# Kernel optimization log

Hardware: AMD Instinct MI355X
Metric: run time of the kernel (lower is better)

## Reference

```python
import jax, jax.numpy as jnp
import numpy as np

SHAPES = [(76, 76), (38, 38), (19, 19), (1, 20)]  # 3 feature levels + task-token pseudo-level
D, HEADS, NLVL, NPTS = 256, 8, 4, 4
DH = D // HEADS
NLAYERS = 6
B = 2
S = sum(h * w for h, w in SHAPES)  # 7601


def _ref_points():
    # valid_ratios == 1 (no padding) -> normalized pixel-center grid per level, concatenated. [S,2] (x,y)
    refs = []
    for H, W in SHAPES:
        ry, rx = jnp.meshgrid(jnp.linspace(0.5, H - 0.5, H) / H,
                              jnp.linspace(0.5, W - 0.5, W) / W, indexing='ij')
        refs.append(jnp.stack([rx.ravel(), ry.ravel()], -1))
    return jnp.concatenate(refs, 0)


def _layer_norm(x, g, b):
    m = x.mean(-1, keepdims=True)
    v = ((x - m) ** 2).mean(-1, keepdims=True)
    return (x - m) * jax.lax.rsqrt(v + 1e-5) * g + b


def _bilinear(val_l, locx, locy, H, W):
    # val_l: [B, H*W, HEADS, DH]; locx/locy: [B,Q,HEADS,P] normalized coords.
    # grid_sample semantics: align_corners=False, zero padding.
    v = val_l.transpose(0, 2, 1, 3)  # [B,Hh,HW,DH]
    x = locx * W - 0.5
    y = locy * H - 0.5
    x0 = jnp.floor(x)
    y0 = jnp.floor(y)
    wx1 = x - x0
    wy1 = y - y0

    def corner(xi, yi, w):
        valid = ((xi >= 0) & (xi <= W - 1) & (yi >= 0) & (yi <= H - 1)).astype(v.dtype)
        idx = (jnp.clip(yi, 0, H - 1) * W + jnp.clip(xi, 0, W - 1)).astype(jnp.int32)
        idx_t = idx.transpose(0, 2, 1, 3)  # [B,Hh,Q,P]
        Bq, Hh, Q, P = idx_t.shape
        g = jnp.take_along_axis(v, idx_t.reshape(Bq, Hh, Q * P)[..., None], axis=2)
        g = g.reshape(Bq, Hh, Q, P, DH)
        return g * (w * valid).transpose(0, 2, 1, 3)[..., None]

    return (corner(x0, y0, (1 - wx1) * (1 - wy1)) + corner(x0 + 1, y0, wx1 * (1 - wy1))
            + corner(x0, y0 + 1, (1 - wx1) * wy1) + corner(x0 + 1, y0 + 1, wx1 * wy1))


def _msdeform(q, x, ref, Woff, boff, Wa, ba, Wv, bv, Wo, bo):
    Bq, Sq, _ = x.shape
    value = (x @ Wv + bv).reshape(Bq, Sq, HEADS, DH)
    off = (q @ Woff + boff).reshape(Bq, Sq, HEADS, NLVL, NPTS, 2)
    attn = jax.nn.softmax((q @ Wa + ba).reshape(Bq, Sq, HEADS, NLVL * NPTS), -1)
    attn = attn.reshape(Bq, Sq, HEADS, NLVL, NPTS)
    acc = jnp.zeros((Bq, HEADS, Sq, DH), x.dtype)
    start = 0
    for l, (H, W) in enumerate(SHAPES):
        n = H * W
        loc = ref[None, :, None, None, :] + off[:, :, :, l] / jnp.asarray([W, H], x.dtype)
        samp = _bilinear(value[:, start:start + n], loc[..., 0], loc[..., 1], H, W)  # [B,Hh,S,P,DH]
        a = attn[:, :, :, l].transpose(0, 2, 1, 3)  # [B,Hh,S,P]
        acc = acc + (samp * a[..., None]).sum(3)
        start += n
    return acc.transpose(0, 2, 1, 3).reshape(Bq, Sq, D) @ Wo + bo


def reference(src0, src1, src2, pos0, pos1, pos2, task_encoding, task_pos_enc, level_embed,
              W_off, b_off, W_attn, b_attn, W_val, b_val, W_out, b_out,
              W1, b1, W2, b2, g1, beta1, g2, beta2):
    srcs, poss = [src0, src1, src2], [pos0, pos1, pos2]
    sf, pf = [], []
    for l in range(3):
        Bq, C, H, W = srcs[l].shape
        sf.append(srcs[l].reshape(Bq, C, H * W).transpose(0, 2, 1))
        pf.append(poss[l].reshape(Bq, C, H * W).transpose(0, 2, 1) + level_embed[l])
    sf.append(task_encoding)
    pf.append(jnp.broadcast_to(task_pos_enc[None], task_encoding.shape))
    x = jnp.concatenate(sf, 1)   # [B,S,D]
    pos = jnp.concatenate(pf, 1)
    ref = _ref_points()
    for i in range(NLAYERS):
        q = x + pos
        x = _layer_norm(x + _msdeform(q, x, ref, W_off[i], b_off[i], W_attn[i], b_attn[i],
                                      W_val[i], b_val[i], W_out[i], b_out[i]), g1[i], beta1[i])
        x = _layer_norm(x + jax.nn.relu(x @ W1[i] + b1[i]) @ W2[i] + b2[i], g2[i], beta2[i])
    return x


def setup_inputs() -> dict:
    key = jax.random.key(0)
    ks = jax.random.split(key, 20)
    d = {}
    for i, (H, W) in enumerate(SHAPES[:3]):
        d[f'src{i}'] = jax.random.normal(ks[i], (B, D, H, W), jnp.float32)
        d[f'pos{i}'] = jax.random.normal(ks[3 + i], (B, D, H, W), jnp.float32) * 0.1
    d['task_encoding'] = jax.random.normal(ks[6], (B, 20, D), jnp.float32)
    d['task_pos_enc'] = jax.random.normal(ks[7], (20, D), jnp.float32) * 0.1
    d['level_embed'] = jax.random.normal(ks[8], (NLVL, D), jnp.float32) * 0.1

    def w(k, shape, s=0.02):
        return jax.random.normal(k, shape, jnp.float32) * s

    d['W_off'] = w(ks[9], (NLAYERS, D, HEADS * NLVL * NPTS * 2), 0.01)
    d['b_off'] = w(ks[10], (NLAYERS, HEADS * NLVL * NPTS * 2), 0.2)
    d['W_attn'] = w(ks[11], (NLAYERS, D, HEADS * NLVL * NPTS))
    d['b_attn'] = jnp.zeros((NLAYERS, HEADS * NLVL * NPTS), jnp.float32)
    d['W_val'] = w(ks[12], (NLAYERS, D, D))
    d['b_val'] = jnp.zeros((NLAYERS, D), jnp.float32)
    d['W_out'] = w(ks[13], (NLAYERS, D, D))
    d['b_out'] = jnp.zeros((NLAYERS, D), jnp.float32)
    d['W1'] = w(ks[14], (NLAYERS, D, 2048))
    d['b1'] = jnp.zeros((NLAYERS, 2048), jnp.float32)
    d['W2'] = w(ks[15], (NLAYERS, 2048, D))
    d['b2'] = jnp.zeros((NLAYERS, D), jnp.float32)
    d['g1'] = jnp.ones((NLAYERS, D), jnp.float32)
    d['beta1'] = jnp.zeros((NLAYERS, D), jnp.float32)
    d['g2'] = jnp.ones((NLAYERS, D), jnp.float32)
    d['beta2'] = jnp.zeros((NLAYERS, D), jnp.float32)
    return d
```

## Files before the change

kernel.cpp:

```cpp
#include <hip/hip_runtime.h>

#define S_TOT 7601
#define BATCH 2
#define BM (BATCH * S_TOT)
#define DMODEL 256

typedef unsigned short bf16;
typedef __attribute__((ext_vector_type(8))) short v8s;
typedef __attribute__((ext_vector_type(4))) float v4f;

__device__ __forceinline__ float b2f(bf16 u) {
    union { unsigned int i; float f; } v;
    v.i = ((unsigned int)u) << 16;
    return v.f;
}
__device__ __forceinline__ bf16 f2b(float f) {
    union { unsigned int i; float f; } v;
    v.f = f;
    unsigned int r = v.i + 0x7FFFu + ((v.i >> 16) & 1u);
    return (bf16)(r >> 16);
}
__device__ __forceinline__ float ldin(const void* p, size_t i, int isf32) {
    return isf32 ? ((const float*)p)[i] : b2f(((const bf16*)p)[i]);
}

#define GLDS16(gp, lp)                                                          \
    __builtin_amdgcn_global_load_lds(                                           \
        (const __attribute__((address_space(1))) unsigned int*)(gp),            \
        (__attribute__((address_space(3))) unsigned int*)(lp), 16, 0, 0)

__device__ __forceinline__ void xcd_remap(int& bx, int& by) {
    int gx = gridDim.x, gy = gridDim.y;
    int nwg = gx * gy;
    int lin = blockIdx.y * gx + blockIdx.x;
    int q = nwg >> 3, r = nwg & 7;
    int xcd = lin & 7, idx = lin >> 3;
    int lin2 = (xcd < r ? xcd * (q + 1) : r * (q + 1) + (xcd - r) * q) + idx;
    bx = lin2 % gx;
    by = lin2 / gx;
}

__global__ void detect_dtype(const unsigned short* __restrict__ src, int* __restrict__ flag) {
    __shared__ int cnt;
    if (threadIdx.x == 0) cnt = 0;
    __syncthreads();
    int local = 0;
    for (int i = threadIdx.x; i < 16384; i += 256) {
        unsigned int e = (src[i] >> 7) & 0xFFu;
        if (e >= 143u) local++;
    }
    atomicAdd(&cnt, local);
    __syncthreads();
    if (threadIdx.x == 0) *flag = (cnt > 200) ? 1 : 0;
}

__global__ void __launch_bounds__(256) pack_level(const void* __restrict__ src,
                                                  const void* __restrict__ pin,
                                                  const void* __restrict__ lemb, int lrow,
                                                  float* __restrict__ x,
                                                  bf16* __restrict__ pout,
                                                  int HW, int start,
                                                  const int* __restrict__ flag) {
    int isf32 = *flag;
    int i = blockIdx.x * 256 + threadIdx.x;
    int total = BATCH * HW * 256;
    if (i >= total) return;
    int c = i & 255;
    int t = i >> 8;
    int s = t % HW;
    int b = t / HW;
    size_t src_idx = ((size_t)b * 256 + c) * HW + s;
    float sv = ldin(src, src_idx, isf32);
    float pv = ldin(pin, src_idx, isf32) + ldin(lemb, (size_t)lrow * 256 + c, isf32);
    size_t o = ((size_t)b * S_TOT + start + s) * 256 + c;
    x[o] = sv;
    pout[o] = f2b(pv);
}

__global__ void __launch_bounds__(256) pack_task(const void* __restrict__ te,
                                                 const void* __restrict__ tpe,
                                                 float* __restrict__ x,
                                                 bf16* __restrict__ pout,
                                                 const int* __restrict__ flag) {
    int isf32 = *flag;
    int i = blockIdx.x * 256 + threadIdx.x;
    int total = BATCH * 20 * 256;
    if (i >= total) return;
    int c = i & 255;
    int t = (i >> 8) % 20;
    int b = (i >> 8) / 20;
    size_t o = ((size_t)b * S_TOT + 7581 + t) * 256 + c;
    x[o] = ldin(te, ((size_t)b * 20 + t) * 256 + c, isf32);
    pout[o] = f2b(ldin(tpe, (size_t)t * 256 + c, isf32));
}

__global__ void __launch_bounds__(256) make_ref(float* __restrict__ ref) {
    int s = blockIdx.x * 256 + threadIdx.x;
    if (s >= S_TOT) return;
    int H, W, st;
    if (s < 5776)      { H = 76; W = 76; st = 0; }
    else if (s < 7220) { H = 38; W = 38; st = 5776; }
    else if (s < 7581) { H = 19; W = 19; st = 7220; }
    else               { H = 1;  W = 20; st = 7581; }
    int r = s - st;
    int i = r / W, j = r % W;
    ref[s * 2 + 0] = (j + 0.5f) / (float)W;
    ref[s * 2 + 1] = (i + 0.5f) / (float)H;
}

__global__ void __launch_bounds__(256) cast_out(const float* __restrict__ x,
                                                void* __restrict__ o, int n,
                                                const int* __restrict__ flag) {
    int isf32 = *flag;
    int i = blockIdx.x * 256 + threadIdx.x;
    if (i >= n) return;
    if (isf32) ((float*)o)[i] = x[i];
    else       ((bf16*)o)[i] = f2b(x[i]);
}

__global__ void __launch_bounds__(256) cvt_x(const float* __restrict__ x,
                                             bf16* __restrict__ xb, int n4) {
    int i = blockIdx.x * 256 + threadIdx.x;
    if (i >= n4) return;
    float4 xv = ((const float4*)x)[i];
    ushort4 xo;
    xo.x = f2b(xv.x); xo.y = f2b(xv.y); xo.z = f2b(xv.z); xo.w = f2b(xv.w);
    ((ushort4*)xb)[i] = xo;
}

__global__ void __launch_bounds__(256) cvt_q(const float* __restrict__ x,
                                             const bf16* __restrict__ pos,
                                             bf16* __restrict__ qb, int n4) {
    int i = blockIdx.x * 256 + threadIdx.x;
    if (i >= n4) return;
    float4 xv = ((const float4*)x)[i];
    ushort4 pv = ((const ushort4*)pos)[i];
    ushort4 qo;
    qo.x = f2b(xv.x + b2f(pv.x));
    qo.y = f2b(xv.y + b2f(pv.y));
    qo.z = f2b(xv.z + b2f(pv.z));
    qo.w = f2b(xv.w + b2f(pv.w));
    ((ushort4*)qb)[i] = qo;
}

__global__ void __launch_bounds__(256) transpose_all(const void* __restrict__ Wv,
                                                     const void* __restrict__ Woff,
                                                     const void* __restrict__ Wa,
                                                     const void* __restrict__ Wo,
                                                     const void* __restrict__ W1,
                                                     const void* __restrict__ W2,
                                                     bf16* __restrict__ Wvt,
                                                     bf16* __restrict__ Wofft,
                                                     bf16* __restrict__ Wat,
                                                     bf16* __restrict__ Wot,
                                                     bf16* __restrict__ W1t,
                                                     bf16* __restrict__ W2t,
                                                     int L, const int* __restrict__ flag) {
    int isf32 = *flag;
    int t = blockIdx.x;
    const void* src; bf16* dst; int K, N; size_t woff;
    if (t < 64)        { src = Wv;   dst = Wvt;   K = 256;  N = 256;  woff = (size_t)L * 65536; }
    else if (t < 128)  { src = Woff; dst = Wofft; K = 256;  N = 256;  woff = (size_t)L * 65536;  t -= 64; }
    else if (t < 160)  { src = Wa;   dst = Wat;   K = 256;  N = 128;  woff = (size_t)L * 32768;  t -= 128; }
    else if (t < 224)  { src = Wo;   dst = Wot;   K = 256;  N = 256;  woff = (size_t)L * 65536;  t -= 160; }
    else if (t < 736)  { src = W1;   dst = W1t;   K = 256;  N = 2048; woff = (size_t)L * 524288; t -= 224; }
    else               { src = W2;   dst = W2t;   K = 2048; N = 256;  woff = (size_t)L * 524288; t -= 736; }
    int ntx = N >> 5;
    int tk = (t / ntx) * 32;
    int tn = (t % ntx) * 32;
    __shared__ float tl[32][33];
    int r = threadIdx.x >> 3;
    int c4 = (threadIdx.x & 7) * 4;
#pragma unroll
    for (int i = 0; i < 4; ++i)
        tl[r][c4 + i] = ldin(src, woff + (size_t)(tk + r) * N + tn + c4 + i, isf32);
    __syncthreads();
#pragma unroll
    for (int i = 0; i < 4; ++i)
        dst[(size_t)(tn + r) * K + tk + c4 + i] = f2b(tl[c4 + i][r]);
}

__global__ void __launch_bounds__(256) mfma_gemm(const bf16* __restrict__ A,
                                                 const bf16* __restrict__ Wt,
                                                 const void* __restrict__ bias, size_t boff,
                                                 bf16* __restrict__ C,
                                                 int M, int N, int K, int relu,
                                                 const int* __restrict__ flag) {
    int isf32 = *flag;
    __shared__ __align__(16) char smem[128 * 136 * 2];
    bf16* Cs = (bf16*)smem;
    int tid = threadIdx.x;
    int lane = tid & 63, wave = tid >> 6;
    int wm = (wave & 1) << 6, wn = (wave >> 1) << 6;
    int bx, by;
    xcd_remap(bx, by);
    int bm = by * 128, bn = bx * 128;
    int q = lane >> 4, l15 = lane & 15;

    v4f acc[4][4];
#pragma unroll
    for (int i = 0; i < 4; ++i)
#pragma unroll
        for (int j = 0; j < 4; ++j) acc[i][j] = (v4f){0.f, 0.f, 0.f, 0.f};

    int r0 = tid >> 2;
    int oct = (tid & 3) * 8;
    int am0 = bm + r0;      if (am0 >= M) am0 = M - 1;
    int am1 = bm + r0 + 64; if (am1 >= M) am1 = M - 1;
    const bf16* ag0 = A + (size_t)am0 * K + oct;
    const bf16* ag1 = A + (size_t)am1 * K + oct;
    const bf16* bg0 = Wt + (size_t)(bn + r0) * K + oct;
    const bf16* bg1 = Wt + (size_t)(bn + r0 + 64) * K + oct;

    int NT = K >> 5;
    {
        bf16* base = (bf16*)smem;
        GLDS16(ag0, base + tid * 8);
        GLDS16(ag1, base + (tid + 256) * 8);
        GLDS16(bg0, base + 4096 + tid * 8);
        GLDS16(bg1, base + 4096 + (tid + 256) * 8);
    }
    __syncthreads();
    for (int it = 0; it < NT; ++it) {
        if (it + 1 < NT) {
            bf16* base = (bf16*)smem + ((it + 1) & 1) * 8192;
            int k0 = (it + 1) << 5;
            GLDS16(ag0 + k0, base + tid * 8);
            GLDS16(ag1 + k0, base + (tid + 256) * 8);
            GLDS16(bg0 + k0, base + 4096 + tid * 8);
            GLDS16(bg1 + k0, base + 4096 + (tid + 256) * 8);
        }
        const bf16* As = (const bf16*)smem + (it & 1) * 8192;
        const bf16* Bs = As + 4096;
        v8s a_frag[4], b_frag[4];
#pragma unroll
        for (int mi = 0; mi < 4; ++mi)
            a_frag[mi] = *(const v8s*)&As[(wm + mi * 16 + l15) * 32 + q * 8];
#pragma unroll
        for (int ni = 0; ni < 4; ++ni)
            b_frag[ni] = *(const v8s*)&Bs[(wn + ni * 16 + l15) * 32 + q * 8];
#pragma unroll
        for (int mi = 0; mi < 4; ++mi)
#pragma unroll
            for (int ni = 0; ni < 4; ++ni)
                acc[mi][ni] = __builtin_amdgcn_mfma_f32_16x16x32_bf16(
                    a_frag[mi], b_frag[ni], acc[mi][ni], 0, 0, 0);
        __syncthreads();
    }

#pragma unroll
    for (int ni = 0; ni < 4; ++ni) {
        int cn = wn + ni * 16 + l15;
        float bv = ldin(bias, boff + bn + cn, isf32);
#pragma unroll
        for (int mi = 0; mi < 4; ++mi) {
#pragma unroll
            for (int r = 0; r < 4; ++r) {
                float v = acc[mi][ni][r] + bv;
                if (relu) v = fmaxf(v, 0.f);
                Cs[(wm + mi * 16 + q * 4 + r) * 136 + cn] = f2b(v);
            }
        }
    }
    __syncthreads();
    {
        int row = tid >> 1, half = tid & 1;
        int gm = bm + row;
        if (gm < M) {
            const bf16* srcp = Cs + row * 136 + half * 64;
            bf16* dstp = C + (size_t)gm * N + bn + half * 64;
#pragma unroll
            for (int i = 0; i < 8; ++i)
                *(uint4*)(dstp + i * 8) = *(const uint4*)(srcp + i * 8);
        }
    }
}

__global__ void __launch_bounds__(256) mfma_gemm64(const bf16* __restrict__ A,
                                                   const bf16* __restrict__ Wt,
                                                   const void* __restrict__ bias, size_t boff,
                                                   bf16* __restrict__ C,
                                                   int M, int N, int K, int relu,
                                                   const int* __restrict__ flag) {
    int isf32 = *flag;
    __shared__ __align__(16) char smem[16384];
    bf16* Cs = (bf16*)smem;
    int tid = threadIdx.x;
    int lane = tid & 63, wave = tid >> 6;
    int wm = (wave & 1) * 32, wn = (wave >> 1) * 32;
    int bx, by;
    xcd_remap(bx, by);
    int bm = by * 64, bn = bx * 64;
    int q = lane >> 4, l15 = lane & 15;

    v4f acc[2][2];
#pragma unroll
    for (int i = 0; i < 2; ++i)
#pragma unroll
        for (int j = 0; j < 2; ++j) acc[i][j] = (v4f){0.f, 0.f, 0.f, 0.f};

    int srow = tid >> 2;
    int oct = (tid & 3) * 8;
    int am = bm + srow; if (am >= M) am = M - 1;
    const bf16* arow = A + (size_t)am * K + oct;
    const bf16* brow = Wt + (size_t)(bn + srow) * K + oct;

    int NT = K >> 5;
    {
        bf16* base = (bf16*)smem;
        GLDS16(arow, base + tid * 8);
        GLDS16(brow, base + 2048 + tid * 8);
    }
    __syncthreads();
    for (int it = 0; it < NT; ++it) {
        if (it + 1 < NT) {
            bf16* base = (bf16*)smem + ((it + 1) & 1) * 4096;
            int k0 = (it + 1) << 5;
            GLDS16(arow + k0, base + tid * 8);
            GLDS16(brow + k0, base + 2048 + tid * 8);
        }
        const bf16* As = (const bf16*)smem + (it & 1) * 4096;
        const bf16* Bs = As + 2048;
        v8s a_frag[2], b_frag[2];
#pragma unroll
        for (int mi = 0; mi < 2; ++mi)
            a_frag[mi] = *(const v8s*)&As[(wm + mi * 16 + l15) * 32 + q * 8];
#pragma unroll
        for (int ni = 0; ni < 2; ++ni)
            b_frag[ni] = *(const v8s*)&Bs[(wn + ni * 16 + l15) * 32 + q * 8];
#pragma unroll
        for (int mi = 0; mi < 2; ++mi)
#pragma unroll
            for (int ni = 0; ni < 2; ++ni)
                acc[mi][ni] = __builtin_amdgcn_mfma_f32_16x16x32_bf16(
                    a_frag[mi], b_frag[ni], acc[mi][ni], 0, 0, 0);
        __syncthreads();
    }

#pragma unroll
    for (int ni = 0; ni < 2; ++ni) {
        int cn = wn + ni * 16 + l15;
        float bv = ldin(bias, boff + bn + cn, isf32);
#pragma unroll
        for (int mi = 0; mi < 2; ++mi) {
#pragma unroll
            for (int r = 0; r < 4; ++r) {
                float v = acc[mi][ni][r] + bv;
                if (relu) v = fmaxf(v, 0.f);
                Cs[(wm + mi * 16 + q * 4 + r) * 72 + cn] = f2b(v);
            }
        }
    }
    __syncthreads();
    {
        int row = tid >> 2, seg = tid & 3;
        int gm = bm + row;
        if (gm < M) {
            const bf16* srcp = Cs + row * 72 + seg * 16;
            bf16* dstp = C + (size_t)gm * N + bn + seg * 16;
            *(uint4*)(dstp) = *(const uint4*)(srcp);
            *(uint4*)(dstp + 8) = *(const uint4*)(srcp + 8);
        }
    }
}

template<typename TA, int ADDPOS, int RELU>
__global__ void __launch_bounds__(256) gemm_bias(const TA* __restrict__ A,
                                                 const bf16* __restrict__ Apos,
                                                 const void* __restrict__ W, size_t woff,
                                                 const void* __restrict__ bias, size_t boff,
                                                 bf16* __restrict__ C,
                                                 int M, int N, int K,
                                                 const int* __restrict__ flag) {
    int isf32 = *flag;
    __shared__ float As[16][65];
    __shared__ float Bs[16][65];
    int tid = threadIdx.x;
    int tx = tid & 15;
    int ty = tid >> 4;
    int bm = blockIdx.y * 64;
    int bn = blockIdx.x * 64;
    float acc[4][4] = {};
    for (int k0 = 0; k0 < K; k0 += 16) {
#pragma unroll
        for (int e = 0; e < 4; ++e) {
            int idx = tid + e * 256;
            int mm = idx >> 4;
            int kk = idx & 15;
            int gm = bm + mm;
            float av = 0.f;
            if (gm < M) {
                size_t ai = (size_t)gm * K + k0 + kk;
                if (sizeof(TA) == 4) av = ((const float*)A)[ai];
                else                 av = b2f(((const bf16*)A)[ai]);
                if (ADDPOS) av += b2f(Apos[ai]);
            }
            As[kk][mm] = av;
        }
#pragma unroll
        for (int e = 0; e < 4; ++e) {
            int idx = tid + e * 256;
            int kk = idx >> 6;
            int nn = idx & 63;
            int gn = bn + nn;
            Bs[kk][nn] = (gn < N) ? ldin(W, woff + (size_t)(k0 + kk) * N + gn, isf32) : 0.f;
        }
        __syncthreads();
#pragma unroll
        for (int kk = 0; kk < 16; ++kk) {
            float a[4], b[4];
#pragma unroll
            for (int i = 0; i < 4; ++i) a[i] = As[kk][ty + 16 * i];
#pragma unroll
            for (int j = 0; j < 4; ++j) b[j] = Bs[kk][tx + 16 * j];
#pragma unroll
            for (int i = 0; i < 4; ++i)
#pragma unroll
                for (int j = 0; j < 4; ++j) acc[i][j] += a[i] * b[j];
        }
        __syncthreads();
    }
#pragma unroll
    for (int i = 0; i < 4; ++i) {
        int gm = bm + ty + 16 * i;
        if (gm >= M) continue;
#pragma unroll
        for (int j = 0; j < 4; ++j) {
            int gn = bn + tx + 16 * j;
            if (gn >= N) continue;
            float v = acc[i][j] + ldin(bias, boff + gn, isf32);
            if (RELU) v = fmaxf(v, 0.f);
            C[(size_t)gm * N + gn] = f2b(v);
        }
    }
}

__global__ void __launch_bounds__(256) msdeform_sample4(const bf16* __restrict__ value,
                                                        const bf16* __restrict__ off,
                                                        const bf16* __restrict__ logits,
                                                        const float* __restrict__ refpts,
                                                        bf16* __restrict__ out) {
    __shared__ float sAttn[4 * 128];
    __shared__ int2 sIW[4 * 520];
    const int LH[4] = {76, 38, 19, 1};
    const int LW[4] = {76, 38, 19, 20};
    const int LS[4] = {0, 5776, 7220, 7581};
    int tid = threadIdx.x;
    int m0 = blockIdx.x * 4;

    for (int i = tid; i < 4 * 128; i += 256) {
        int r = i >> 7, li = i & 127;
        int m = m0 + r;
        int mc = (m < BM) ? m : BM - 1;
        sAttn[i] = b2f(logits[(size_t)mc * 128 + li]);
    }
    __syncthreads();
    if (tid < 32) {
        float* g = sAttn + tid * 16;
        float mx = -1e30f;
#pragma unroll
        for (int i = 0; i < 16; ++i) mx = fmaxf(mx, g[i]);
        float e[16], sm = 0.f;
#pragma unroll
        for (int i = 0; i < 16; ++i) { e[i] = __expf(g[i] - mx); sm += e[i]; }
        float inv = 1.f / sm;
#pragma unroll
        for (int i = 0; i < 16; ++i) g[i] = e[i] * inv;
    }
    __syncthreads();
    for (int i = tid; i < 4 * 128; i += 256) {
        int r = i >> 7, oi = i & 127;
        int m = m0 + r;
        int mc = (m < BM) ? m : BM - 1;
        int b = mc / S_TOT;
        int s = mc - b * S_TOT;
        int h = oi >> 4;
        int l = (oi >> 2) & 3;
        int H = LH[l], W = LW[l], st = LS[l];
        float fW = (float)W, fH = (float)H;
        float refx = refpts[s * 2 + 0];
        float refy = refpts[s * 2 + 1];
        ushort2 ov = *(const ushort2*)(off + (size_t)mc * 256 + oi * 2);
        float a = sAttn[r * 128 + oi];
        float xpix = (refx + b2f(ov.x) / fW) * fW - 0.5f;
        float ypix = (refy + b2f(ov.y) / fH) * fH - 0.5f;
        float x0f = floorf(xpix), y0f = floorf(ypix);
        int x0 = (int)x0f, y0 = (int)y0f;
        float wx1 = xpix - x0f, wy1 = ypix - y0f;
        float wx0 = 1.f - wx1, wy0 = 1.f - wy1;
        int vb = b * (S_TOT * 256) + h * 32;
        int base = r * 520 + h * 65 + (oi & 15) * 4;
#pragma unroll
        for (int c = 0; c < 4; ++c) {
            int cx = c & 1, cy = c >> 1;
            int xi = x0 + cx, yi = y0 + cy;
            float w = (cx ? wx1 : wx0) * (cy ? wy1 : wy0) * a;
            bool valid = (xi >= 0) && (xi <= W - 1) && (yi >= 0) && (yi <= H - 1);
            int xic = min(max(xi, 0), W - 1), yic = min(max(yi, 0), H - 1);
            int2 d;
            d.x = vb + (st + yic * W + xic) * 256;
            d.y = __float_as_int(valid ? w : 0.f);
            sIW[base + c] = d;
        }
    }
    __syncthreads();
    int r = tid >> 6, u = tid & 63;
    int h = u >> 3, d4 = (u & 7) * 4;
    int m = m0 + r;
    int cb = r * 520 + h * 65;
    float acc0 = 0.f, acc1 = 0.f, acc2 = 0.f, acc3 = 0.f;
#pragma unroll 8
    for (int c = 0; c < 64; ++c) {
        int2 p = sIW[cb + c];
        float w = __int_as_float(p.y);
        ushort4 v = *(const ushort4*)(value + p.x + d4);
        acc0 += w * b2f(v.x);
        acc1 += w * b2f(v.y);
        acc2 += w * b2f(v.z);
        acc3 += w * b2f(v.w);
    }
    if (m < BM) {
        ushort4 o;
        o.x = f2b(acc0); o.y = f2b(acc1); o.z = f2b(acc2); o.w = f2b(acc3);
        *(ushort4*)(out + (size_t)m * 256 + h * 32 + d4) = o;
    }
}

__global__ void __launch_bounds__(256) residual_ln4(float* __restrict__ x,
                                                    const bf16* __restrict__ y,
                                                    const void* __restrict__ g, size_t goff,
                                                    const void* __restrict__ beta, size_t boff,
                                                    const int* __restrict__ flag,
                                                    bf16* __restrict__ xb,
                                                    const bf16* __restrict__ pos,
                                                    bf16* __restrict__ qb) {
    int isf32 = *flag;
    int tid = threadIdx.x;
    int r = tid >> 6, lane = tid & 63;
    int m = blockIdx.x * 4 + r;
    if (m >= BM) return;
    size_t o = (size_t)m * 256 + lane * 4;
    float4 xv = *(const float4*)(x + o);
    ushort4 yv = *(const ushort4*)(y + o);
    float r0 = xv.x + b2f(yv.x), r1 = xv.y + b2f(yv.y);
    float r2 = xv.z + b2f(yv.z), r3 = xv.w + b2f(yv.w);
    float sum = r0 + r1 + r2 + r3;
#pragma unroll
    for (int ofs = 32; ofs > 0; ofs >>= 1) sum += __shfl_xor(sum, ofs);
    float mean = sum * (1.f / 256.f);
    float d0 = r0 - mean, d1 = r1 - mean, d2 = r2 - mean, d3 = r3 - mean;
    float vv = d0 * d0 + d1 * d1 + d2 * d2 + d3 * d3;
#pragma unroll
    for (int ofs = 32; ofs > 0; ofs >>= 1) vv += __shfl_xor(vv, ofs);
    float rstd = rsqrtf(vv * (1.f / 256.f) + 1e-5f);
    int c = lane * 4;
    float o0 = d0 * rstd * ldin(g, goff + c + 0, isf32) + ldin(beta, boff + c + 0, isf32);
    float o1 = d1 * rstd * ldin(g, goff + c + 1, isf32) + ldin(beta, boff + c + 1, isf32);
    float o2 = d2 * rstd * ldin(g, goff + c + 2, isf32) + ldin(beta, boff + c + 2, isf32);
    float o3 = d3 * rstd * ldin(g, goff + c + 3, isf32) + ldin(beta, boff + c + 3, isf32);
    *(float4*)(x + o) = make_float4(o0, o1, o2, o3);
    if (xb) {
        ushort4 xo;
        xo.x = f2b(o0); xo.y = f2b(o1); xo.z = f2b(o2); xo.w = f2b(o3);
        *(ushort4*)(xb + o) = xo;
    }
    if (qb) {
        ushort4 pv = *(const ushort4*)(pos + o);
        ushort4 qo;
        qo.x = f2b(o0 + b2f(pv.x));
        qo.y = f2b(o1 + b2f(pv.y));
        qo.z = f2b(o2 + b2f(pv.z));
        qo.w = f2b(o3 + b2f(pv.w));
        *(ushort4*)(qb + o) = qo;
    }
}

extern "C" void kernel_launch(void* const* d_in, const int* in_sizes, int n_in,
                              void* d_out, int out_size, void* d_ws, size_t ws_size,
                              hipStream_t stream) {
    (void)in_sizes; (void)n_in; (void)out_size;
    const size_t MS = (size_t)BM * DMODEL;

    char* base = (char*)d_ws;
    int* flag    = (int*)base;    base += 256;
    float* x     = (float*)base;  base += MS * 4;
    bf16* value  = (bf16*)base;   base += MS * 2;
    bf16* attnl  = (bf16*)base;   base += (size_t)BM * 128 * 2;
    bf16* pos    = (bf16*)base;   base += MS * 2;
    bf16* offms  = (bf16*)base;   base += MS * 2;
    bf16* yb     = (bf16*)base;   base += MS * 2;
    size_t base_used = (size_t)(base - (char*)d_ws);

    bf16* xb = (bf16*)base;
    size_t need_fast = base_used + MS * 2
                     + (size_t)2048 * 256 * 2 * 2
                     + (size_t)256 * 256 * 2 * 3
                     + (size_t)128 * 256 * 2
                     + (size_t)S_TOT * 2 * 4 + 1024;
    bool FAST = ws_size >= need_fast;

    bf16 *W1t = nullptr, *W2t = nullptr, *Wvt = nullptr, *Wofft = nullptr, *Wot = nullptr, *Wat = nullptr;
    float* ref;
    bf16* hiddenF = nullptr;
    bool FULLH = false;
    if (FAST) {
        char* p = (char*)xb + MS * 2;
        W1t = (bf16*)p;   p += (size_t)2048 * 256 * 2;
        W2t = (bf16*)p;   p += (size_t)2048 * 256 * 2;
        Wvt = (bf16*)p;   p += (size_t)256 * 256 * 2;
        Wofft = (bf16*)p; p += (size_t)256 * 256 * 2;
        Wot = (bf16*)p;   p += (size_t)256 * 256 * 2;
        Wat = (bf16*)p;   p += (size_t)128 * 256 * 2;
        ref = (float*)p;  p += (size_t)S_TOT * 2 * 4;
        size_t used = (size_t)(p - (char*)d_ws);
        used = (used + 255) & ~(size_t)255;
        if (ws_size >= used + (size_t)BM * 2048 * 2) {
            hiddenF = (bf16*)((char*)d_ws + used);
            FULLH = true;
        }
    } else {
        ref = (float*)base;
    }

    bf16* hidden = FULLH ? hiddenF : value;
    const int CH = FULLH ? BM : 2816;

    detect_dtype<<<1, 256, 0, stream>>>((const unsigned short*)d_in[0], flag);

    {
        int HW0 = 76 * 76, HW1 = 38 * 38, HW2 = 19 * 19;
        int n0 = BATCH * HW0 * 256, n1 = BATCH * HW1 * 256, n2 = BATCH * HW2 * 256;
        pack_level<<<(n0 + 255) / 256, 256, 0, stream>>>(d_in[0], d_in[1], d_in[8], 0, x, pos, HW0, 0, flag);
        pack_level<<<(n1 + 255) / 256, 256, 0, stream>>>(d_in[2], d_in[3], d_in[8], 1, x, pos, HW1, 5776, flag);
        pack_level<<<(n2 + 255) / 256, 256, 0, stream>>>(d_in[4], d_in[5], d_in[8], 2, x, pos, HW2, 7220, flag);
        int nt = BATCH * 20 * 256;
        pack_task<<<(nt + 255) / 256, 256, 0, stream>>>(d_in[6], d_in[7], x, pos, flag);
        make_ref<<<(S_TOT + 255) / 256, 256, 0, stream>>>(ref);
    }

    const int GM64 = (BM + 63) / 64;
    const int GR4 = (BM + 3) / 4;
    const int n4 = (int)(MS / 4);

    if (FAST) {
        cvt_x<<<(n4 + 255) / 256, 256, 0, stream>>>(x, xb, n4);
        cvt_q<<<(n4 + 255) / 256, 256, 0, stream>>>(x, pos, yb, n4);
    }

    for (int L = 0; L < 6; ++L) {
        size_t oW256 = (size_t)L * 256 * 256, ob256 = (size_t)L * 256;
        size_t oW128 = (size_t)L * 256 * 128, ob128 = (size_t)L * 128;
        size_t oW1   = (size_t)L * 256 * 2048, ob1  = (size_t)L * 2048;
        size_t oW2   = (size_t)L * 2048 * 256;

        if (FAST) {
            transpose_all<<<1248, 256, 0, stream>>>(d_in[13], d_in[9], d_in[11], d_in[15], d_in[17], d_in[19],
                                                    Wvt, Wofft, Wat, Wot, W1t, W2t, L, flag);
            bf16* qb = yb;
            mfma_gemm64<<<dim3(4, GM64), 256, 0, stream>>>(xb, Wvt, d_in[14], ob256, value, BM, 256, 256, 0, flag);
            mfma_gemm64<<<dim3(4, GM64), 256, 0, stream>>>(qb, Wofft, d_in[10], ob256, offms, BM, 256, 256, 0, flag);
            mfma_gemm64<<<dim3(2, GM64), 256, 0, stream>>>(qb, Wat, d_in[12], ob128, attnl, BM, 128, 256, 0, flag);

            msdeform_sample4<<<GR4, 256, 0, stream>>>(value, offms, attnl, ref, offms);

            mfma_gemm64<<<dim3(4, GM64), 256, 0, stream>>>(offms, Wot, d_in[16], ob256, yb, BM, 256, 256, 0, flag);
            residual_ln4<<<GR4, 256, 0, stream>>>(x, yb, d_in[21], ob256, d_in[22], ob256, flag, xb, nullptr, nullptr);

            for (int r0 = 0; r0 < BM; r0 += CH) {
                int mc = BM - r0 < CH ? BM - r0 : CH;
                int gmc128 = (mc + 127) / 128;
                int gmc64 = (mc + 63) / 64;
                mfma_gemm<<<dim3(16, gmc128), 256, 0, stream>>>(xb + (size_t)r0 * 256, W1t, d_in[18], ob1,
                                                                hidden, mc, 2048, 256, 1, flag);
                mfma_gemm64<<<dim3(4, gmc64), 256, 0, stream>>>(hidden, W2t, d_in[20], ob256,
                                                                yb + (size_t)r0 * 256, mc, 256, 2048, 0, flag);
            }
            residual_ln4<<<GR4, 256, 0, stream>>>(x, yb, d_in[23], ob256, d_in[24], ob256, flag, xb,
                                                  (L < 5) ? pos : nullptr, (L < 5) ? yb : nullptr);
        } else {
            dim3 g256(4, GM64);
            dim3 g128(2, GM64);
            gemm_bias<float, 0, 0><<<g256, 256, 0, stream>>>(x, nullptr, d_in[13], oW256, d_in[14], ob256,
                                                             value, BM, 256, 256, flag);
            gemm_bias<float, 1, 0><<<g256, 256, 0, stream>>>(x, pos, d_in[9], oW256, d_in[10], ob256,
                                                             offms, BM, 256, 256, flag);
            gemm_bias<float, 1, 0><<<g128, 256, 0, stream>>>(x, pos, d_in[11], oW128, d_in[12], ob128,
                                                             attnl, BM, 128, 256, flag);
            msdeform_sample4<<<GR4, 256, 0, stream>>>(value, offms, attnl, ref, offms);
            gemm_bias<bf16, 0, 0><<<g256, 256, 0, stream>>>(offms, nullptr, d_in[15], oW256, d_in[16], ob256,
                                                            yb, BM, 256, 256, flag);
            residual_ln4<<<GR4, 256, 0, stream>>>(x, yb, d_in[21], ob256, d_in[22], ob256, flag, nullptr, nullptr, nullptr);
            for (int r0 = 0; r0 < BM; r0 += CH) {
                int mc = BM - r0 < CH ? BM - r0 : CH;
                dim3 gh(32, (mc + 63) / 64);
                dim3 go(4, (mc + 63) / 64);
                gemm_bias<float, 0, 1><<<gh, 256, 0, stream>>>(x + (size_t)r0 * 256, nullptr, d_in[17], oW1,
                                                               d_in[18], ob1, hidden, mc, 2048, 256, flag);
                gemm_bias<bf16, 0, 0><<<go, 256, 0, stream>>>(hidden, nullptr, d_in[19], oW2, d_in[20], ob256,
                                                              yb + (size_t)r0 * 256, mc, 256, 2048, flag);
            }
            residual_ln4<<<GR4, 256, 0, stream>>>(x, yb, d_in[23], ob256, d_in[24], ob256, flag, nullptr, nullptr, nullptr);
        }
    }

    cast_out<<<((int)MS + 255) / 256, 256, 0, stream>>>(x, d_out, (int)MS, flag);
}
```

Baseline: 1.259 ms.

## Replace GEMM kernels with single-buffered 128x64 tile, two-wave variant

Introduces a 128-row by 64-column tile GEMM with two waves per block and uses it for the value, offset, output-projection, and both FFN GEMMs. Larger M tiles improve weight reuse for the N=256 GEMMs compared with the 64x64 kernel. The smaller LDS footprint and block size allow more resident blocks per CU. The double-buffered prefetch is dropped in favor of a load-sync-compute loop, which risks exposing global load latency.

```diff
diff --git a/kernel.cpp b/kernel.cpp
--- a/kernel.cpp
+++ b/kernel.cpp
@@ -180,21 +180,23 @@
         dst[(size_t)(tn + r) * K + tk + c4 + i] = f2b(tl[c4 + i][r]);
 }
 
-__global__ void __launch_bounds__(256) mfma_gemm(const bf16* __restrict__ A,
-                                                 const bf16* __restrict__ Wt,
-                                                 const void* __restrict__ bias, size_t boff,
-                                                 bf16* __restrict__ C,
-                                                 int M, int N, int K, int relu,
-                                                 const int* __restrict__ flag) {
-    int isf32 = *flag;
-    __shared__ __align__(16) char smem[128 * 136 * 2];
+__global__ void __launch_bounds__(128) mfma_gemm12864(const bf16* __restrict__ A,
+                                                      const bf16* __restrict__ Wt,
+                                                      const void* __restrict__ bias, size_t boff,
+                                                      bf16* __restrict__ C,
+                                                      int M, int N, int K, int relu,
+                                                      const int* __restrict__ flag) {
+    int isf32 = *flag;
+    __shared__ __align__(16) char smem[18432];
+    bf16* As = (bf16*)smem;
+    bf16* Bs = (bf16*)smem + 4096;
     bf16* Cs = (bf16*)smem;
     int tid = threadIdx.x;
     int lane = tid & 63, wave = tid >> 6;
-    int wm = (wave & 1) << 6, wn = (wave >> 1) << 6;
+    int wm = wave << 6;
     int bx, by;
     xcd_remap(bx, by);
-    int bm = by * 128, bn = bx * 128;
+    int bm = by * 128, bn = bx * 64;
     int q = lane >> 4, l15 = lane & 15;
 
     v4f acc[4][4];
@@ -205,40 +207,31 @@
 
     int r0 = tid >> 2;
     int oct = (tid & 3) * 8;
-    int am0 = bm + r0;      if (am0 >= M) am0 = M - 1;
-    int am1 = bm + r0 + 64; if (am1 >= M) am1 = M - 1;
-    const bf16* ag0 = A + (size_t)am0 * K + oct;
-    const bf16* ag1 = A + (size_t)am1 * K + oct;
+    const bf16* ag[4];
+#pragma unroll
+    for (int p = 0; p < 4; ++p) {
+        int am = bm + r0 + 32 * p;
+        if (am >= M) am = M - 1;
+        ag[p] = A + (size_t)am * K + oct;
+    }
     const bf16* bg0 = Wt + (size_t)(bn + r0) * K + oct;
-    const bf16* bg1 = Wt + (size_t)(bn + r0 + 64) * K + oct;
-
-    int NT = K >> 5;
-    {
-        bf16* base = (bf16*)smem;
-        GLDS16(ag0, base + tid * 8);
-        GLDS16(ag1, base + (tid + 256) * 8);
-        GLDS16(bg0, base + 4096 + tid * 8);
-        GLDS16(bg1, base + 4096 + (tid + 256) * 8);
-    }
-    __syncthreads();
-    for (int it = 0; it < NT; ++it) {
-        if (it + 1 < NT) {
-            bf16* base = (bf16*)smem + ((it + 1) & 1) * 8192;
-            int k0 = (it + 1) << 5;
-            GLDS16(ag0 + k0, base + tid * 8);
-            GLDS16(ag1 + k0, base + (tid + 256) * 8);
-            GLDS16(bg0 + k0, base + 4096 + tid * 8);
-            GLDS16(bg1 + k0, base + 4096 + (tid + 256) * 8);
-        }
-        const bf16* As = (const bf16*)smem + (it & 1) * 8192;
-        const bf16* Bs = As + 4096;
+    const bf16* bg1 = Wt + (size_t)(bn + r0 + 32) * K + oct;
+
+    for (int k0 = 0; k0 < K; k0 += 32) {
+        GLDS16(ag[0] + k0, As + tid * 8);
+        GLDS16(ag[1] + k0, As + (tid + 128) * 8);
+        GLDS16(ag[2] + k0, As + (tid + 256) * 8);
+        GLDS16(ag[3] + k0, As + (tid + 384) * 8);
+        GLDS16(bg0 + k0, Bs + tid * 8);
+        GLDS16(bg1 + k0, Bs + (tid + 128) * 8);
+        __syncthreads();
         v8s a_frag[4], b_frag[4];
 #pragma unroll
         for (int mi = 0; mi < 4; ++mi)
             a_frag[mi] = *(const v8s*)&As[(wm + mi * 16 + l15) * 32 + q * 8];
 #pragma unroll
         for (int ni = 0; ni < 4; ++ni)
-            b_frag[ni] = *(const v8s*)&Bs[(wn + ni * 16 + l15) * 32 + q * 8];
+            b_frag[ni] = *(const v8s*)&Bs[(ni * 16 + l15) * 32 + q * 8];
 #pragma unroll
         for (int mi = 0; mi < 4; ++mi)
 #pragma unroll
@@ -250,7 +243,7 @@
 
 #pragma unroll
     for (int ni = 0; ni < 4; ++ni) {
-        int cn = wn + ni * 16 + l15;
+        int cn = ni * 16 + l15;
         float bv = ldin(bias, boff + bn + cn, isf32);
 #pragma unroll
         for (int mi = 0; mi < 4; ++mi) {
@@ -258,20 +251,19 @@
             for (int r = 0; r < 4; ++r) {
                 float v = acc[mi][ni][r] + bv;
                 if (relu) v = fmaxf(v, 0.f);
-                Cs[(wm + mi * 16 + q * 4 + r) * 136 + cn] = f2b(v);
+                Cs[(wm + mi * 16 + q * 4 + r) * 72 + cn] = f2b(v);
             }
         }
     }
     __syncthreads();
     {
-        int row = tid >> 1, half = tid & 1;
-        int gm = bm + row;
+        int gm = bm + tid;
         if (gm < M) {
-            const bf16* srcp = Cs + row * 136 + half * 64;
-            bf16* dstp = C + (size_t)gm * N + bn + half * 64;
-#pragma unroll
-            for (int i = 0; i < 8; ++i)
-                *(uint4*)(dstp + i * 8) = *(const uint4*)(srcp + i * 8);
+            const bf16* srcp = Cs + tid * 72;
+            bf16* dstp = C + (size_t)gm * N + bn;
+#pragma unroll
+            for (int seg = 0; seg < 8; ++seg)
+                *(uint4*)(dstp + seg * 8) = *(const uint4*)(srcp + seg * 8);
         }
     }
 }
@@ -639,6 +631,7 @@
     }
 
     const int GM64 = (BM + 63) / 64;
+    const int GM128 = (BM + 127) / 128;
     const int GR4 = (BM + 3) / 4;
     const int n4 = (int)(MS / 4);
 
@@ -657,23 +650,22 @@
             transpose_all<<<1248, 256, 0, stream>>>(d_in[13], d_in[9], d_in[11], d_in[15], d_in[17], d_in[19],
                                                     Wvt, Wofft, Wat, Wot, W1t, W2t, L, flag);
             bf16* qb = yb;
-            mfma_gemm64<<<dim3(4, GM64), 256, 0, stream>>>(xb, Wvt, d_in[14], ob256, value, BM, 256, 256, 0, flag);
-            mfma_gemm64<<<dim3(4, GM64), 256, 0, stream>>>(qb, Wofft, d_in[10], ob256, offms, BM, 256, 256, 0, flag);
+            mfma_gemm12864<<<dim3(4, GM128), 128, 0, stream>>>(xb, Wvt, d_in[14], ob256, value, BM, 256, 256, 0, flag);
+            mfma_gemm12864<<<dim3(4, GM128), 128, 0, stream>>>(qb, Wofft, d_in[10], ob256, offms, BM, 256, 256, 0, flag);
             mfma_gemm64<<<dim3(2, GM64), 256, 0, stream>>>(qb, Wat, d_in[12], ob128, attnl, BM, 128, 256, 0, flag);
 
             msdeform_sample4<<<GR4, 256, 0, stream>>>(value, offms, attnl, ref, offms);
 
-            mfma_gemm64<<<dim3(4, GM64), 256, 0, stream>>>(offms, Wot, d_in[16], ob256, yb, BM, 256, 256, 0, flag);
+            mfma_gemm12864<<<dim3(4, GM128), 128, 0, stream>>>(offms, Wot, d_in[16], ob256, yb, BM, 256, 256, 0, flag);
             residual_ln4<<<GR4, 256, 0, stream>>>(x, yb, d_in[21], ob256, d_in[22], ob256, flag, xb, nullptr, nullptr);
 
             for (int r0 = 0; r0 < BM; r0 += CH) {
                 int mc = BM - r0 < CH ? BM - r0 : CH;
-                int gmc128 = (mc + 127) / 128;
-                int gmc64 = (mc + 63) / 64;
-                mfma_gemm<<<dim3(16, gmc128), 256, 0, stream>>>(xb + (size_t)r0 * 256, W1t, d_in[18], ob1,
-                                                                hidden, mc, 2048, 256, 1, flag);
-                mfma_gemm64<<<dim3(4, gmc64), 256, 0, stream>>>(hidden, W2t, d_in[20], ob256,
-                                                                yb + (size_t)r0 * 256, mc, 256, 2048, 0, flag);
+                int gmc = (mc + 127) / 128;
+                mfma_gemm12864<<<dim3(32, gmc), 128, 0, stream>>>(xb + (size_t)r0 * 256, W1t, d_in[18], ob1,
+                                                                  hidden, mc, 2048, 256, 1, flag);
+                mfma_gemm12864<<<dim3(4, gmc), 128, 0, stream>>>(hidden, W2t, d_in[20], ob256,
+                                                                 yb + (size_t)r0 * 256, mc, 256, 2048, 0, flag);
             }
             residual_ln4<<<GR4, 256, 0, stream>>>(x, yb, d_in[23], ob256, d_in[24], ob256, flag, xb,
                                                   (L < 5) ? pos : nullptr, (L < 5) ? yb : nullptr);
```

Result: slower. 1.455 ms (+15.6%).
